# Optimization experiments

Hardware: AMD Instinct MI355X
Metric: run time of the kernel (lower is better)

The kernel has to match this reference:

```python
import jax, jax.numpy as jnp
import numpy as np

N_EMBED = 1024
NUM_EXPERTS = 8
TOP_K = 2


def setup_inputs() -> dict:
    key = jax.random.key(0)
    ks = jax.random.split(key, 7)
    d, e, h = N_EMBED, NUM_EXPERTS, 4 * N_EMBED
    s = 1.0 / np.sqrt(d)
    sh = 1.0 / np.sqrt(h)
    return {
        "x": jax.random.normal(ks[0], (4, 2048, d), dtype=jnp.float32),
        "Wg": jax.random.uniform(ks[1], (d, e), jnp.float32, -s, s),
        "bg": jax.random.uniform(ks[2], (e,), jnp.float32, -s, s),
        "W1": jax.random.uniform(ks[3], (e, d, h), jnp.float32, -s, s),
        "b1": jax.random.uniform(ks[4], (e, h), jnp.float32, -s, s),
        "W2": jax.random.uniform(ks[5], (e, h, d), jnp.float32, -sh, sh),
        "b2": jax.random.uniform(ks[6], (e, d), jnp.float32, -sh, sh),
    }


def reference(x, Wg, bg, W1, b1, W2, b2):
    # Gating: softmax over ALL experts, then top-k (no renormalization, matching original)
    logits = jnp.einsum("bsd,de->bse", x, Wg) + bg
    probs = jax.nn.softmax(logits, axis=-1)
    weights, indices = jax.lax.top_k(probs, TOP_K)  # [B,S,K]

    out = jnp.zeros_like(x)
    for ei in range(NUM_EXPERTS):
        # combined gate weight for this expert per token [B,S]
        gate = jnp.sum(jnp.where(indices == ei, weights, 0.0), axis=-1)
        hid = jax.nn.relu(jnp.einsum("bsd,dh->bsh", x, W1[ei]) + b1[ei])
        eo = jnp.einsum("bsh,hd->bsd", hid, W2[ei]) + b2[ei]
        out = out + gate[..., None] * eo
    return out
```

## Files before the change

### kernel.cpp

```cpp
#include <hip/hip_runtime.h>
#include <hip/hip_bf16.h>
#include <stdint.h>
#include <math.h>


#define TOKENS   8192
#define DIM      1024
#define HIDN     4096
#define NEXP     8
#define PAIRS    (TOKENS * 2)
#define MAXROWS  (PAIRS + NEXP * 64)
#define MAXTILES 136
#define NHB      128

typedef __attribute__((ext_vector_type(8))) short short8;
typedef __attribute__((ext_vector_type(4))) float f32x4;

#define AS1 __attribute__((address_space(1)))
#define AS3 __attribute__((address_space(3)))

__device__ inline short bf16b(float f) {
    __hip_bfloat16 h = __float2bfloat16(f);
    return *reinterpret_cast<short*>(&h);
}

__global__ __launch_bounds__(256) void gating_kernel(
    const float* __restrict__ x, const float* __restrict__ Wg,
    const float* __restrict__ bg,
    int* __restrict__ topk_e, float* __restrict__ topk_w)
{
    int t    = blockIdx.x * 4 + (threadIdx.x >> 6);
    int lane = threadIdx.x & 63;
    if (t >= TOKENS) return;
    const float* xr = x + (size_t)t * DIM;

    float acc[8];
#pragma unroll
    for (int e = 0; e < 8; ++e) acc[e] = 0.f;

#pragma unroll 4
    for (int j = 0; j < DIM / 64; ++j) {
        int idx = j * 64 + lane;
        float xv = xr[idx];
        const float* wr = Wg + (size_t)idx * 8;
        float4 w0 = *(const float4*)(wr);
        float4 w1 = *(const float4*)(wr + 4);
        acc[0] += xv * w0.x; acc[1] += xv * w0.y;
        acc[2] += xv * w0.z; acc[3] += xv * w0.w;
        acc[4] += xv * w1.x; acc[5] += xv * w1.y;
        acc[6] += xv * w1.z; acc[7] += xv * w1.w;
    }
#pragma unroll
    for (int off = 32; off > 0; off >>= 1)
#pragma unroll
        for (int e = 0; e < 8; ++e) acc[e] += __shfl_down(acc[e], off);

    if (lane == 0) {
        float lg[8];
#pragma unroll
        for (int e = 0; e < 8; ++e) lg[e] = acc[e] + bg[e];
        float mx = lg[0];
#pragma unroll
        for (int e = 1; e < 8; ++e) mx = fmaxf(mx, lg[e]);
        float p[8]; float s = 0.f;
#pragma unroll
        for (int e = 0; e < 8; ++e) { p[e] = expf(lg[e] - mx); s += p[e]; }
        int e0 = 0;
#pragma unroll
        for (int e = 1; e < 8; ++e) if (p[e] > p[e0]) e0 = e;
        int e1 = -1;
#pragma unroll
        for (int e = 0; e < 8; ++e)
            if (e != e0 && (e1 < 0 || p[e] > p[e1])) e1 = e;
        float inv = 1.f / s;
        topk_e[t * 2 + 0] = e0;  topk_w[t * 2 + 0] = p[e0] * inv;
        topk_e[t * 2 + 1] = e1;  topk_w[t * 2 + 1] = p[e1] * inv;
    }
}

__global__ __launch_bounds__(128) void hist_kernel(
    const int* __restrict__ topk_e, int* __restrict__ hist)
{
    __shared__ int h[8];
    int t = threadIdx.x, b = blockIdx.x;
    if (t < 8) h[t] = 0;
    __syncthreads();
    atomicAdd(&h[topk_e[b * 128 + t]], 1);
    __syncthreads();
    if (t < 8) hist[b * 8 + t] = h[t];
}

__global__ __launch_bounds__(128) void plan_kernel(
    const int* __restrict__ hist, int* __restrict__ base,
    int* __restrict__ tile_e, int* __restrict__ tile_row0, int* __restrict__ n_tiles)
{
    __shared__ int sx[8][NHB];
    __shared__ int tot[8];
    __shared__ int segs[8];
    __shared__ int wtot[2];
    int t = threadIdx.x, lane = t & 63, wid = t >> 6;
#pragma unroll
    for (int e = 0; e < 8; ++e) {
        int hv = hist[t * 8 + e];
        int v = hv;
#pragma unroll
        for (int off = 1; off < 64; off <<= 1) {
            int n = __shfl_up(v, off);
            if (lane >= off) v += n;
        }
        if (lane == 63) wtot[wid] = v;
        __syncthreads();
        int incl = v + (wid ? wtot[0] : 0);
        sx[e][t] = incl - hv;
        if (t == NHB - 1) tot[e] = incl;
        __syncthreads();
    }
    if (t == 0) {
        int off = 0, nt = 0;
        for (int e = 0; e < 8; ++e) {
            segs[e] = off;
            int tl = (tot[e] + 127) >> 7;
            for (int i = 0; i < tl; ++i) { tile_e[nt] = e; tile_row0[nt] = off + i * 128; ++nt; }
            off += tl * 128;
        }
        *n_tiles = nt;
    }
    __syncthreads();
#pragma unroll
    for (int e = 0; e < 8; ++e) base[t * 8 + e] = segs[e] + sx[e][t];
}

__global__ __launch_bounds__(128) void gather_rank(
    const int* __restrict__ topk_e, const float* __restrict__ topk_w,
    const int* __restrict__ base, int* __restrict__ pair_row,
    int* __restrict__ row_token, float* __restrict__ row_gate)
{
    __shared__ int cnt[8];
    int t = threadIdx.x, b = blockIdx.x;
    if (t < 8) cnt[t] = 0;
    __syncthreads();
    int pr = b * 128 + t;
    int e  = topk_e[pr];
    int lr = atomicAdd(&cnt[e], 1);
    int row = base[b * 8 + e] + lr;
    pair_row[pr]   = row;
    row_token[row] = pr >> 1;
    row_gate[row]  = topk_w[pr];
}

__global__ __launch_bounds__(256) void scatter_copy(
    const float* __restrict__ x, const int* __restrict__ pair_row,
    __hip_bfloat16* __restrict__ xe)
{
    int b = blockIdx.x;
    int wv = threadIdx.x >> 6, lane = threadIdx.x & 63;
#pragma unroll 4
    for (int i = 0; i < 16; ++i) {
        int p   = b * 64 + i * 4 + wv;
        int row = pair_row[p];
        int tok = p >> 1;
        const float* xr = x + (size_t)tok * DIM;
        __hip_bfloat16* xo = xe + (size_t)row * DIM;
        int idx = lane * 16;
        float4 v0 = *(const float4*)(xr + idx);
        float4 v1 = *(const float4*)(xr + idx + 4);
        float4 v2 = *(const float4*)(xr + idx + 8);
        float4 v3 = *(const float4*)(xr + idx + 12);
        short8 o0, o1;
        o0[0] = bf16b(v0.x); o0[1] = bf16b(v0.y); o0[2] = bf16b(v0.z); o0[3] = bf16b(v0.w);
        o0[4] = bf16b(v1.x); o0[5] = bf16b(v1.y); o0[6] = bf16b(v1.z); o0[7] = bf16b(v1.w);
        o1[0] = bf16b(v2.x); o1[1] = bf16b(v2.y); o1[2] = bf16b(v2.z); o1[3] = bf16b(v2.w);
        o1[4] = bf16b(v3.x); o1[5] = bf16b(v3.y); o1[6] = bf16b(v3.z); o1[7] = bf16b(v3.w);
        *(short8*)(xo + idx)     = o0;
        *(short8*)(xo + idx + 8) = o1;
    }
}

__global__ __launch_bounds__(256) void transpose_cvt_kernel(
    const float* __restrict__ src, __hip_bfloat16* __restrict__ dst,
    int rows, int cols)
{
    __shared__ float tile[32][33];
    int e  = blockIdx.z;
    const float* s = src + (size_t)e * rows * cols;
    __hip_bfloat16* d = dst + (size_t)e * rows * cols;
    int c0 = blockIdx.x * 32, r0 = blockIdx.y * 32;
    int tx = threadIdx.x & 31, ty = threadIdx.x >> 5;
#pragma unroll
    for (int j = 0; j < 4; ++j) {
        int rr = ty + j * 8;
        tile[rr][tx] = s[(size_t)(r0 + rr) * cols + c0 + tx];
    }
    __syncthreads();
    int t  = threadIdx.x;
    int cr = t >> 3;
    int g  = t & 7;
    ushort o[4];
#pragma unroll
    for (int j = 0; j < 4; ++j) o[j] = (ushort)bf16b(tile[g * 4 + j][cr]);
    *(uint2*)(d + (size_t)(c0 + cr) * rows + r0 + g * 4) = *(uint2*)o;
}

template <int MODE>
__global__ __launch_bounds__(256) void moe_gemm(
    const __hip_bfloat16* __restrict__ A,
    const __hip_bfloat16* __restrict__ Bw,
    const float* __restrict__ bias,
    const int* __restrict__ tile_e, const int* __restrict__ tile_row0,
    const int* __restrict__ n_tiles,
    int K, int N,
    __hip_bfloat16* __restrict__ hid,
    const int* __restrict__ row_token, const float* __restrict__ row_gate,
    float* __restrict__ out)
{
    int tidx = blockIdx.x;
    if (tidx >= *n_tiles) return;
    int e  = tile_e[tidx];
    int m0 = tile_row0[tidx];
    int n0 = blockIdx.y * 128;
    const __hip_bfloat16* Bb = Bw + (size_t)e * N * K;

    __shared__ __hip_bfloat16 lA[128 * 64];
    __shared__ __hip_bfloat16 lB[128 * 64];

    int tid  = threadIdx.x;
    int w    = tid >> 6;
    int l    = tid & 63;
    int r    = l & 15;
    int quad = l >> 4;
    int subrow = l >> 3;
    int cswz   = ((l & 7) ^ subrow) * 16;
    int wm = (w >> 1) * 64;
    int wn = (w & 1) * 64;

    const f32x4 fzero = {0.f, 0.f, 0.f, 0.f};
    f32x4 acc[4][4];
#pragma unroll
    for (int mi = 0; mi < 4; ++mi)
#pragma unroll
        for (int ni = 0; ni < 4; ++ni) acc[mi][ni] = fzero;

    const size_t ldb = (size_t)K * 2;
    int rsw = (r & 7);

    for (int k0 = 0; k0 < K; k0 += 64) {
#pragma unroll
        for (int i = 0; i < 4; ++i) {
            int chunk = i * 4 + w;
            int rowA  = chunk * 8 + subrow;
            const char* gA = (const char*)A + (size_t)(m0 + rowA) * ldb + (size_t)k0 * 2 + cswz;
            const char* gB = (const char*)Bb + (size_t)(n0 + rowA) * ldb + (size_t)k0 * 2 + cswz;
            char* sA = (char*)lA + chunk * 1024;
            char* sB = (char*)lB + chunk * 1024;
            __builtin_amdgcn_global_load_lds((const AS1 void*)gA, (AS3 void*)sA, 16, 0, 0);
            __builtin_amdgcn_global_load_lds((const AS1 void*)gB, (AS3 void*)sB, 16, 0, 0);
        }
        __syncthreads();
#pragma unroll
        for (int kk = 0; kk < 2; ++kk) {
            int slot = ((kk * 4 + quad) ^ rsw) * 16;
            short8 aF[4], bF[4];
#pragma unroll
            for (int mi = 0; mi < 4; ++mi) {
                int row = wm + mi * 16 + r;
                aF[mi] = *(const short8*)((const char*)lA + row * 128 + slot);
            }
#pragma unroll
            for (int ni = 0; ni < 4; ++ni) {
                int row = wn + ni * 16 + r;
                bF[ni] = *(const short8*)((const char*)lB + row * 128 + slot);
            }
#pragma unroll
            for (int mi = 0; mi < 4; ++mi)
#pragma unroll
                for (int ni = 0; ni < 4; ++ni)
                    acc[mi][ni] = __builtin_amdgcn_mfma_f32_16x16x32_bf16(
                        aF[mi], bF[ni], acc[mi][ni], 0, 0, 0);
        }
        __syncthreads();
    }

    if (MODE == 1) {
#pragma unroll
        for (int mi = 0; mi < 4; ++mi)
#pragma unroll
            for (int i = 0; i < 4; ++i) {
                int row = m0 + wm + mi * 16 + quad * 4 + i;
                size_t rb = (size_t)row * N;
#pragma unroll
                for (int ni = 0; ni < 4; ++ni) {
                    int col = n0 + wn + ni * 16 + r;
                    float v = acc[mi][ni][i] + bias[e * N + col];
                    hid[rb + col] = __float2bfloat16(fmaxf(v, 0.f));
                }
            }
    } else {
#pragma unroll
        for (int mi = 0; mi < 4; ++mi)
#pragma unroll
            for (int i = 0; i < 4; ++i) {
                int row = m0 + wm + mi * 16 + quad * 4 + i;
                int token = row_token[row];
                if ((unsigned)token < (unsigned)TOKENS) {
                    float g = row_gate[row];
                    float* orow = out + (size_t)token * DIM;
#pragma unroll
                    for (int ni = 0; ni < 4; ++ni) {
                        int col = n0 + wn + ni * 16 + r;
                        float v = acc[mi][ni][i] + bias[e * N + col];
                        atomicAdd(orow + col, g * v);
                    }
                }
            }
    }
}

extern "C" void kernel_launch(void* const* d_in, const int* in_sizes, int n_in,
                              void* d_out, int out_size, void* d_ws, size_t ws_size,
                              hipStream_t stream) {
    const float* x  = (const float*)d_in[0];
    const float* Wg = (const float*)d_in[1];
    const float* bg = (const float*)d_in[2];
    const float* W1 = (const float*)d_in[3];
    const float* b1 = (const float*)d_in[4];
    const float* W2 = (const float*)d_in[5];
    const float* b2 = (const float*)d_in[6];
    float* out = (float*)d_out;

    char* w = (char*)d_ws;
    int*   n_tiles   = (int*)(w + 0);
    int*   tile_e    = (int*)(w + 256);
    int*   tile_row0 = (int*)(w + 2048);
    int*   hist      = (int*)(w + 4096);
    int*   base      = (int*)(w + 8192);
    int*   topk_e    = (int*)(w + 12288);
    float* topk_w    = (float*)(w + 77824);
    int*   pair_row  = (int*)(w + 143360);
    int*   row_token = (int*)(w + 208896);
    float* row_gate  = (float*)(w + 278528);
    __hip_bfloat16* xe  = (__hip_bfloat16*)(w + 348160);
    __hip_bfloat16* hid = (__hip_bfloat16*)(w + 35999744ULL);
    __hip_bfloat16* W1b = (__hip_bfloat16*)(w + 178606080ULL);
    __hip_bfloat16* W2b = (__hip_bfloat16*)(w + 245714944ULL);

    hipMemsetAsync(out, 0, (size_t)out_size * sizeof(float), stream);

    gating_kernel<<<TOKENS / 4, 256, 0, stream>>>(x, Wg, bg, topk_e, topk_w);
    hist_kernel<<<NHB, 128, 0, stream>>>(topk_e, hist);
    plan_kernel<<<1, 128, 0, stream>>>(hist, base, tile_e, tile_row0, n_tiles);
    gather_rank<<<NHB, 128, 0, stream>>>(topk_e, topk_w, base, pair_row,
                                         row_token, row_gate);
    scatter_copy<<<256, 256, 0, stream>>>(x, pair_row, xe);

    transpose_cvt_kernel<<<dim3(HIDN / 32, DIM / 32, NEXP), 256, 0, stream>>>(W1, W1b, DIM, HIDN);
    transpose_cvt_kernel<<<dim3(DIM / 32, HIDN / 32, NEXP), 256, 0, stream>>>(W2, W2b, HIDN, DIM);

    moe_gemm<1><<<dim3(MAXTILES, HIDN / 128), 256, 0, stream>>>(
        xe, W1b, b1, tile_e, tile_row0, n_tiles, DIM, HIDN,
        hid, nullptr, nullptr, nullptr);
    moe_gemm<2><<<dim3(MAXTILES, DIM / 128), 256, 0, stream>>>(
        hid, W2b, b2, tile_e, tile_row0, n_tiles, HIDN, DIM,
        nullptr, row_token, row_gate, out);
}
```

Before: 848.1 us.

## Double K-step per barrier, vectorize transpose loads, swizzle tile order, init row buffers

The grouped GEMM now loads a 128-wide K slice per iteration into two LDS halves, halving the number of barrier pairs, at the cost of twice the LDS per block and possibly lower occupancy. Tile indices are remapped so consecutive blocks are strided across the tile list, which is meant to spread experts across CUs and improve cache locality. The weight transpose kernel uses float4 loads with one row per thread group instead of a four-pass scalar loop. Row token and gate buffers are now cleared with memsets so padding rows are well defined.

```diff
diff --git a/kernel.cpp b/kernel.cpp
--- a/kernel.cpp
+++ b/kernel.cpp
@@ -185,14 +185,13 @@
     const float* s = src + (size_t)e * rows * cols;
     __hip_bfloat16* d = dst + (size_t)e * rows * cols;
     int c0 = blockIdx.x * 32, r0 = blockIdx.y * 32;
-    int tx = threadIdx.x & 31, ty = threadIdx.x >> 5;
-#pragma unroll
-    for (int j = 0; j < 4; ++j) {
-        int rr = ty + j * 8;
-        tile[rr][tx] = s[(size_t)(r0 + rr) * cols + c0 + tx];
-    }
-    __syncthreads();
     int t  = threadIdx.x;
+    int ty = t >> 3;
+    int tx = (t & 7) * 4;
+    float4 v = *(const float4*)(s + (size_t)(r0 + ty) * cols + c0 + tx);
+    tile[ty][tx + 0] = v.x; tile[ty][tx + 1] = v.y;
+    tile[ty][tx + 2] = v.z; tile[ty][tx + 3] = v.w;
+    __syncthreads();
     int cr = t >> 3;
     int g  = t & 7;
     ushort o[4];
@@ -213,15 +212,16 @@
     const int* __restrict__ row_token, const float* __restrict__ row_gate,
     float* __restrict__ out)
 {
-    int tidx = blockIdx.x;
+    int bx   = blockIdx.x;
+    int tidx = (bx & 7) * (MAXTILES / 8) + (bx >> 3);
     if (tidx >= *n_tiles) return;
     int e  = tile_e[tidx];
     int m0 = tile_row0[tidx];
     int n0 = blockIdx.y * 128;
     const __hip_bfloat16* Bb = Bw + (size_t)e * N * K;
 
-    __shared__ __hip_bfloat16 lA[128 * 64];
-    __shared__ __hip_bfloat16 lB[128 * 64];
+    __shared__ __hip_bfloat16 lA[2 * 128 * 64];
+    __shared__ __hip_bfloat16 lB[2 * 128 * 64];
 
     int tid  = threadIdx.x;
     int w    = tid >> 6;
@@ -232,6 +232,7 @@
     int cswz   = ((l & 7) ^ subrow) * 16;
     int wm = (w >> 1) * 64;
     int wn = (w & 1) * 64;
+    int rsw = r & 7;
 
     const f32x4 fzero = {0.f, 0.f, 0.f, 0.f};
     f32x4 acc[4][4];
@@ -241,34 +242,37 @@
         for (int ni = 0; ni < 4; ++ni) acc[mi][ni] = fzero;
 
     const size_t ldb = (size_t)K * 2;
-    int rsw = (r & 7);
-
-    for (int k0 = 0; k0 < K; k0 += 64) {
+
+    for (int k0 = 0; k0 < K; k0 += 128) {
 #pragma unroll
         for (int i = 0; i < 4; ++i) {
-            int chunk = i * 4 + w;
-            int rowA  = chunk * 8 + subrow;
-            const char* gA = (const char*)A + (size_t)(m0 + rowA) * ldb + (size_t)k0 * 2 + cswz;
-            const char* gB = (const char*)Bb + (size_t)(n0 + rowA) * ldb + (size_t)k0 * 2 + cswz;
-            char* sA = (char*)lA + chunk * 1024;
-            char* sB = (char*)lB + chunk * 1024;
-            __builtin_amdgcn_global_load_lds((const AS1 void*)gA, (AS3 void*)sA, 16, 0, 0);
-            __builtin_amdgcn_global_load_lds((const AS1 void*)gB, (AS3 void*)sB, 16, 0, 0);
+            int c   = i * 4 + w;
+            int row = c * 8 + subrow;
+            const char* gA = (const char*)A  + (size_t)(m0 + row) * ldb + (size_t)k0 * 2;
+            const char* gB = (const char*)Bb + (size_t)(n0 + row) * ldb + (size_t)k0 * 2;
+#pragma unroll
+            for (int h = 0; h < 2; ++h) {
+                char* sA = (char*)lA + h * 16384 + c * 1024;
+                char* sB = (char*)lB + h * 16384 + c * 1024;
+                __builtin_amdgcn_global_load_lds((const AS1 void*)(gA + h * 128 + cswz), (AS3 void*)sA, 16, 0, 0);
+                __builtin_amdgcn_global_load_lds((const AS1 void*)(gB + h * 128 + cswz), (AS3 void*)sB, 16, 0, 0);
+            }
         }
         __syncthreads();
 #pragma unroll
-        for (int kk = 0; kk < 2; ++kk) {
-            int slot = ((kk * 4 + quad) ^ rsw) * 16;
+        for (int kk = 0; kk < 4; ++kk) {
+            int hoff = (kk >> 1) * 16384;
+            int slot = ((((kk & 1) * 4) + quad) ^ rsw) * 16;
             short8 aF[4], bF[4];
 #pragma unroll
             for (int mi = 0; mi < 4; ++mi) {
                 int row = wm + mi * 16 + r;
-                aF[mi] = *(const short8*)((const char*)lA + row * 128 + slot);
+                aF[mi] = *(const short8*)((const char*)lA + hoff + row * 128 + slot);
             }
 #pragma unroll
             for (int ni = 0; ni < 4; ++ni) {
                 int row = wn + ni * 16 + r;
-                bF[ni] = *(const short8*)((const char*)lB + row * 128 + slot);
+                bF[ni] = *(const short8*)((const char*)lB + hoff + row * 128 + slot);
             }
 #pragma unroll
             for (int mi = 0; mi < 4; ++mi)
@@ -344,6 +348,8 @@
     __hip_bfloat16* W2b = (__hip_bfloat16*)(w + 245714944ULL);
 
     hipMemsetAsync(out, 0, (size_t)out_size * sizeof(float), stream);
+    hipMemsetAsync(row_token, 0xFF, 69632, stream);
+    hipMemsetAsync(row_gate, 0, 69632, stream);
 
     gating_kernel<<<TOKENS / 4, 256, 0, stream>>>(x, Wg, bg, topk_e, topk_w);
     hist_kernel<<<NHB, 128, 0, stream>>>(topk_e, hist);
```

Result: slower. 908.0 us (+7.1%).
